# Kernel optimization log

Measured on AMD Instinct MI355X. Metric: run time of the kernel, lower is better.

Reference implementation:

```python
import jax, jax.numpy as jnp
import numpy as np

H = 2048

def _lstm_layer(x, W_ih, W_hh, b_ih, b_hh):
    # x: [B,T,I]; W_ih: [4H,I]; W_hh: [4H,H]; gate order i,f,g,o (PyTorch)
    B = x.shape[0]
    x_proj = jnp.einsum('bti,gi->btg', x, W_ih) + b_ih + b_hh  # [B,T,4H]
    def step(carry, xt):
        h, c = carry
        gates = xt + h @ W_hh.T                     # [B,4H]
        i, f, g, o = jnp.split(gates, 4, axis=-1)
        i = jax.nn.sigmoid(i); f = jax.nn.sigmoid(f)
        g = jnp.tanh(g);       o = jax.nn.sigmoid(o)
        c = f * c + i * g
        h = o * jnp.tanh(c)
        return (h, c), h
    h0 = jnp.zeros((B, H), x.dtype)
    c0 = jnp.zeros((B, H), x.dtype)
    _, ys = jax.lax.scan(step, (h0, c0), x_proj.transpose(1, 0, 2))
    return ys.transpose(1, 0, 2)  # [B,T,H]

def setup_inputs() -> dict:
    key = jax.random.key(0)
    ks = jax.random.split(key, 16)
    B, T, I, O = 16, 128, 128, 1
    s = 1.0 / np.sqrt(H)
    def u(k, shape):
        return jax.random.uniform(k, shape, jnp.float32, -s, s)
    inp = {"x": jax.random.normal(ks[0], (B, T, I), jnp.float32)}
    in_dims = [I, H, H]
    for l in range(3):
        inp[f"W_ih{l}"] = u(ks[1 + 4 * l], (4 * H, in_dims[l]))
        inp[f"W_hh{l}"] = u(ks[2 + 4 * l], (4 * H, H))
        inp[f"b_ih{l}"] = u(ks[3 + 4 * l], (4 * H,))
        inp[f"b_hh{l}"] = u(ks[4 + 4 * l], (4 * H,))
    inp["W_out"] = u(ks[13], (O, H))
    inp["b_out"] = u(ks[14], (O,))
    return inp

def reference(x, W_ih0, W_hh0, b_ih0, b_hh0,
              W_ih1, W_hh1, b_ih1, b_hh1,
              W_ih2, W_hh2, b_ih2, b_hh2,
              W_out, b_out):
    h = _lstm_layer(x, W_ih0, W_hh0, b_ih0, b_hh0)
    h = _lstm_layer(h, W_ih1, W_hh1, b_ih1, b_hh1)
    h = _lstm_layer(h, W_ih2, W_hh2, b_ih2, b_hh2)
    return h @ W_out.T + b_out  # [B,T,O]
```

## Files before the change

### kernel.cpp

```cpp
#include <hip/hip_runtime.h>
#include <hip/hip_fp16.h>
#include <cstdint>
#include <cstddef>


typedef __attribute__((ext_vector_type(8))) _Float16 fp16x8;
typedef __attribute__((ext_vector_type(4))) float    f32x4;

#define HDIM  2048
#define GATES 8192
#define BATCH 16
#define TSEQ  128
#define NTOK  2048
#define RED_ST 17
#define HSLOT 128
#define HSTEP_ELEMS 32768
#define FLAG_STRIDE 16
#define NFLAG_COPY 4
#define FB_OFF (NFLAG_COPY * 256 * FLAG_STRIDE)

union HU { _Float16 f; unsigned short u; };

__device__ __forceinline__ float sigmoidf_(float x) { return 1.f / (1.f + __expf(-x)); }
__device__ __forceinline__ float tanhf_(float x) {
    float e2 = __expf(2.f * x);
    return 1.f - 2.f / (e2 + 1.f);
}

__global__ __launch_bounds__(256) void cvt_f32_f16_kernel(const float* __restrict__ in,
                                                          _Float16* __restrict__ out, int n8) {
    int i = blockIdx.x * 256 + threadIdx.x;
    if (i >= n8) return;
    const float4* p = (const float4*)in + (size_t)i * 2;
    float4 a = p[0], b = p[1];
    fp16x8 v;
    v[0] = (_Float16)a.x; v[1] = (_Float16)a.y; v[2] = (_Float16)a.z; v[3] = (_Float16)a.w;
    v[4] = (_Float16)b.x; v[5] = (_Float16)b.y; v[6] = (_Float16)b.z; v[7] = (_Float16)b.w;
    ((fp16x8*)out)[i] = v;
}

__global__ __launch_bounds__(256) void xproj_gemm_kernel(
        const _Float16* __restrict__ A, const _Float16* __restrict__ Ah,
        const _Float16* __restrict__ W,
        const float* __restrict__ bih, const float* __restrict__ bhh,
        float* __restrict__ xp, int K) {
    __shared__ _Float16 As[128 * 64];
    __shared__ _Float16 Bs[128 * 64];
    const int tid  = threadIdx.x;
    const int lane = tid & 63;
    const int wave = tid >> 6;
    const int n0 = blockIdx.x * 128;
    const int m0 = blockIdx.y * 128;
    const int srow = tid >> 3;
    const int scol = (tid & 7) * 8;
    const int wr = (wave >> 1) * 64;
    const int wc = (wave & 1) * 64;
    const int lr = lane & 15;
    const int lk = (lane >> 4) * 8;

    f32x4 acc[4][4] = {};

    const int nk = K >> 6;
    for (int kt = 0; kt < nk; ++kt) {
        if (kt) __syncthreads();
        const int k0 = kt * 64;
#pragma unroll
        for (int cc = 0; cc < 4; ++cc) {
            const int row = cc * 32 + srow;
            const _Float16* ga;
            if (Ah) {
                const int m = m0 + row, b = m >> 7, tt = m & 127;
                ga = Ah + (size_t)(tt + 1) * HSTEP_ELEMS + (size_t)(k0 + scol) * 16 + b * 8;
            } else {
                ga = A + (size_t)(m0 + row) * K + k0 + scol;
            }
            const _Float16* gb = W + (size_t)(n0 + row) * K + k0 + scol;
            __builtin_amdgcn_global_load_lds(
                (const __attribute__((address_space(1))) void*)ga,
                (__attribute__((address_space(3))) void*)(As + cc * 2048 + wave * 512), 16, 0, 0);
            __builtin_amdgcn_global_load_lds(
                (const __attribute__((address_space(1))) void*)gb,
                (__attribute__((address_space(3))) void*)(Bs + cc * 2048 + wave * 512), 16, 0, 0);
        }
        __syncthreads();
#pragma unroll
        for (int s = 0; s < 2; ++s) {
            fp16x8 af[4], bf[4];
#pragma unroll
            for (int mi = 0; mi < 4; ++mi)
                af[mi] = *(const fp16x8*)(As + (wr + mi * 16 + lr) * 64 + s * 32 + lk);
#pragma unroll
            for (int ni = 0; ni < 4; ++ni)
                bf[ni] = *(const fp16x8*)(Bs + (wc + ni * 16 + lr) * 64 + s * 32 + lk);
#pragma unroll
            for (int mi = 0; mi < 4; ++mi)
#pragma unroll
                for (int ni = 0; ni < 4; ++ni)
                    acc[mi][ni] = __builtin_amdgcn_mfma_f32_16x16x32_f16(
                        af[mi], bf[ni], acc[mi][ni], 0, 0, 0);
        }
    }
    const int rb = (lane >> 4) * 4;
#pragma unroll
    for (int ni = 0; ni < 4; ++ni) {
        const int n = n0 + wc + ni * 16 + lr;
        const float bias = bih[n] + bhh[n];
#pragma unroll
        for (int mi = 0; mi < 4; ++mi) {
#pragma unroll
            for (int r = 0; r < 4; ++r) {
                const int m = m0 + wr + mi * 16 + rb + r;
                const int b = m >> 7, t = m & 127;
                xp[((size_t)t * BATCH + b) * GATES + n] = acc[mi][ni][r] + bias;
            }
        }
    }
}

__global__ __launch_bounds__(256, 1) void lstm_scan_kernel(
        const float* __restrict__ Whh,
        const float* __restrict__ xp,
        _Float16* __restrict__ hstep,
        int* __restrict__ flags,
        int flag_base) {
    __builtin_amdgcn_fence(__ATOMIC_ACQUIRE, "agent");

    __shared__ float red[2][8 * 16 * RED_ST];

    const int tid  = threadIdx.x;
    const int lane = tid & 63;
    const int wave = tid >> 6;
    const int blk  = blockIdx.x;
    const int h0   = blk * 8;
    const int ln15 = lane & 15;
    const int kl   = (lane >> 4) * 8;
    const int kbase = wave * 512;

    const int rq = ln15 >> 3, rj = ln15 & 7;
    const float* w0 = Whh + ((size_t)rq * HDIM + h0 + rj) * HDIM;
    const float* w1 = Whh + ((size_t)(rq + 2) * HDIM + h0 + rj) * HDIM;
    fp16x8 b0[16], b1[16];
#pragma unroll
    for (int s = 0; s < 16; ++s) {
        const int k = kbase + s * 32 + kl;
        float4 a0 = *(const float4*)(w0 + k), a1 = *(const float4*)(w0 + k + 4);
        float4 c0 = *(const float4*)(w1 + k), c1 = *(const float4*)(w1 + k + 4);
        fp16x8 v;
        v[0] = (_Float16)a0.x; v[1] = (_Float16)a0.y; v[2] = (_Float16)a0.z; v[3] = (_Float16)a0.w;
        v[4] = (_Float16)a1.x; v[5] = (_Float16)a1.y; v[6] = (_Float16)a1.z; v[7] = (_Float16)a1.w;
        b0[s] = v;
        v[0] = (_Float16)c0.x; v[1] = (_Float16)c0.y; v[2] = (_Float16)c0.z; v[3] = (_Float16)c0.w;
        v[4] = (_Float16)c1.x; v[5] = (_Float16)c1.y; v[6] = (_Float16)c1.z; v[7] = (_Float16)c1.w;
        b1[s] = v;
    }
    float c_state = 0.f;
    const int uh = tid & 7, ub = tid >> 3;

    const int pidx = ((blk & 3) << 8) | (wave << 6) | lane;
    const int* fa = flags + (size_t)pidx * FLAG_STRIDE;
    const int* fb = fa + FB_OFF;

    __syncthreads();

    for (int t = 0; t < TSEQ; ++t) {
        if (t) {
            while (__hip_atomic_load(fa, __ATOMIC_RELAXED, __HIP_MEMORY_SCOPE_AGENT) < flag_base + t ||
                   __hip_atomic_load(fb, __ATOMIC_RELAXED, __HIP_MEMORY_SCOPE_AGENT) < flag_base + t) {}
        }
        asm volatile("" ::: "memory");
        const _Float16* hsrc = hstep + (size_t)t * HSTEP_ELEMS;

        fp16x8 af[16];
#pragma unroll
        for (int s = 0; s < 16; ++s) {
            const int k = kbase + s * 32 + kl;
            af[s] = *(const fp16x8*)(hsrc + (size_t)k * 16 + ln15 * 8);
        }

        float xi = 0.f, xf = 0.f, xg = 0.f, xo = 0.f;
        if (tid < 128) {
            const float* xpt = xp + ((size_t)t * BATCH + ub) * GATES + h0 + uh;
            xi = xpt[0];
            xf = xpt[HDIM];
            xg = xpt[2 * HDIM];
            xo = xpt[3 * HDIM];
        }

        f32x4 a0e = {0.f,0.f,0.f,0.f}, a0o = {0.f,0.f,0.f,0.f};
        f32x4 a1e = {0.f,0.f,0.f,0.f}, a1o = {0.f,0.f,0.f,0.f};
#pragma unroll
        for (int s = 0; s < 16; s += 2) {
            a0e = __builtin_amdgcn_mfma_f32_16x16x32_f16(af[s],     b0[s],     a0e, 0, 0, 0);
            a1e = __builtin_amdgcn_mfma_f32_16x16x32_f16(af[s],     b1[s],     a1e, 0, 0, 0);
            a0o = __builtin_amdgcn_mfma_f32_16x16x32_f16(af[s + 1], b0[s + 1], a0o, 0, 0, 0);
            a1o = __builtin_amdgcn_mfma_f32_16x16x32_f16(af[s + 1], b1[s + 1], a1o, 0, 0, 0);
        }
        f32x4 acc0 = a0e + a0o;
        f32x4 acc1 = a1e + a1o;
        {
            float* r0 = red[t & 1] + ((wave * 2 + 0) * 16 + ln15) * RED_ST + (lane >> 4) * 4;
            float* r1 = red[t & 1] + ((wave * 2 + 1) * 16 + ln15) * RED_ST + (lane >> 4) * 4;
#pragma unroll
            for (int i = 0; i < 4; ++i) { r0[i] = acc0[i]; r1[i] = acc1[i]; }
        }
        __syncthreads();
        asm volatile("" ::: "memory");

        if (tid < 128) {
            const float* redp = red[t & 1];
            float ip = xi, fp_ = xf, gp = xg, op = xo;
#pragma unroll
            for (int w = 0; w < 4; ++w) {
                ip  += redp[((w * 2 + 0) * 16 + uh    ) * RED_ST + ub];
                fp_ += redp[((w * 2 + 0) * 16 + uh + 8) * RED_ST + ub];
                gp  += redp[((w * 2 + 1) * 16 + uh    ) * RED_ST + ub];
                op  += redp[((w * 2 + 1) * 16 + uh + 8) * RED_ST + ub];
            }
            float ig = sigmoidf_(ip), fg = sigmoidf_(fp_), og = sigmoidf_(op);
            float gg = tanhf_(gp);
            c_state = fg * c_state + ig * gg;
            float hv = og * tanhf_(c_state);
            HU cv; cv.f = (_Float16)hv;
            unsigned v  = cv.u;
            unsigned v1 = __shfl_down(v, 1, 64);
            unsigned v2 = __shfl_down(v, 2, 64);
            unsigned v3 = __shfl_down(v, 3, 64);
            if ((tid & 3) == 0) {
                unsigned long long pk = (unsigned long long)v
                                      | ((unsigned long long)v1 << 16)
                                      | ((unsigned long long)v2 << 32)
                                      | ((unsigned long long)v3 << 48);
                unsigned long long* dst = (unsigned long long*)
                    (hstep + (size_t)(t + 1) * HSTEP_ELEMS + blk * HSLOT + ub * 8 + uh);
                __hip_atomic_store(dst, pk, __ATOMIC_RELAXED, __HIP_MEMORY_SCOPE_AGENT);
            }
            if (t < TSEQ - 1) {
                asm volatile("s_waitcnt vmcnt(0)" ::: "memory");
                if (lane == 0) {
                    int* base = flags + (wave ? FB_OFF : 0);
#pragma unroll
                    for (int c = 0; c < NFLAG_COPY; ++c)
                        __hip_atomic_store(base + (size_t)((c << 8) | blk) * FLAG_STRIDE,
                                           flag_base + t + 1,
                                           __ATOMIC_RELAXED, __HIP_MEMORY_SCOPE_AGENT);
                }
            }
        }
    }
}

__global__ __launch_bounds__(256) void outproj_kernel(
        const _Float16* __restrict__ hstep, const float* __restrict__ Wout,
        const float* __restrict__ bout, float* __restrict__ out) {
    const int lane = threadIdx.x & 63;
    const int wave = threadIdx.x >> 6;
    const int tok = blockIdx.x * 4 + wave;
    const int b = tok >> 7, t = tok & 127;
    const _Float16* h = hstep + (size_t)(t + 1) * HSTEP_ELEMS + b * 8;
    float acc = 0.f;
#pragma unroll
    for (int c = 0; c < 4; ++c) {
        const int k = c * 512 + lane * 8;
        fp16x8 hv = *(const fp16x8*)(h + (size_t)k * 16);
        const float* w = Wout + k;
#pragma unroll
        for (int i = 0; i < 8; ++i) acc += (float)hv[i] * w[i];
    }
#pragma unroll
    for (int off = 32; off > 0; off >>= 1) acc += __shfl_down(acc, off, 64);
    if (lane == 0) out[tok] = acc + bout[0];
}

extern "C" void kernel_launch(void* const* d_in, const int* in_sizes, int n_in,
                              void* d_out, int out_size, void* d_ws, size_t ws_size,
                              hipStream_t stream) {
    (void)in_sizes; (void)n_in; (void)out_size; (void)ws_size;
    const float* x       = (const float*)d_in[0];
    const float* Wih[3]  = {(const float*)d_in[1], (const float*)d_in[5], (const float*)d_in[9]};
    const float* Whh[3]  = {(const float*)d_in[2], (const float*)d_in[6], (const float*)d_in[10]};
    const float* bih[3]  = {(const float*)d_in[3], (const float*)d_in[7], (const float*)d_in[11]};
    const float* bhh[3]  = {(const float*)d_in[4], (const float*)d_in[8], (const float*)d_in[12]};
    const float* Wout    = (const float*)d_in[13];
    const float* bout    = (const float*)d_in[14];
    float* out = (float*)d_out;

    char* ws = (char*)d_ws;
    size_t off = 0;
    auto carve = [&](size_t bytes) {
        char* p = ws + off;
        off += (bytes + 255) & ~(size_t)255;
        return p;
    };
    _Float16* wih16 = (_Float16*)carve((size_t)GATES * 2048 * 2);
    float*    xp    = (float*)   carve((size_t)TSEQ * GATES * BATCH * 4);
    _Float16* xh    = (_Float16*)carve((size_t)NTOK * 128 * 2);
    _Float16* hstep = (_Float16*)carve((size_t)(TSEQ + 1) * HSTEP_ELEMS * 2);
    int*      flags = (int*)     carve((size_t)2 * NFLAG_COPY * 256 * FLAG_STRIDE * 4);

    hipMemsetAsync(flags, 0, (size_t)2 * NFLAG_COPY * 256 * FLAG_STRIDE * 4, stream);
    hipMemsetAsync(hstep, 0, HSTEP_ELEMS * 2, stream);

    {
        int n8 = NTOK * 128 / 8;
        cvt_f32_f16_kernel<<<(n8 + 255) / 256, 256, 0, stream>>>(x, xh, n8);
    }

    const int Kl[3] = {128, 2048, 2048};
    for (int l = 0; l < 3; ++l) {
        int n8 = GATES * Kl[l] / 8;
        cvt_f32_f16_kernel<<<(n8 + 255) / 256, 256, 0, stream>>>(Wih[l], wih16, n8);
        dim3 ggrid(GATES / 128, NTOK / 128);
        xproj_gemm_kernel<<<ggrid, 256, 0, stream>>>(
            l == 0 ? xh : nullptr, l == 0 ? nullptr : hstep,
            wih16, bih[l], bhh[l], xp, Kl[l]);
        lstm_scan_kernel<<<256, 256, 0, stream>>>(Whh[l], xp, hstep, flags, l * TSEQ);
    }
    outproj_kernel<<<NTOK / 4, 256, 0, stream>>>(hstep, Wout, bout, out);
}
```

Measured before the change: 1.728 ms.

## Replace flag-based step barrier with sentinel-filled hidden-state ring polling

Drops the separate per-block flag counters and the vmcnt wait before the flag stores. Consumers now poll the hidden-state data directly: each 64-bit chunk is pre-filled with an fp16 infinity sentinel and reloaded until it is overwritten. This removes a store-to-flag round trip on every timestep of the serial recurrence. In exchange it adds a ring prefill kernel per layer, alternates two ring buffers between layers, and assumes a real h value never equals the sentinel.

Result: slower. 2.252 ms (+30.3%).

```diff
diff --git a/kernel.cpp b/kernel.cpp
--- a/kernel.cpp
+++ b/kernel.cpp
@@ -5,6 +5,7 @@
 
 
 typedef __attribute__((ext_vector_type(8))) _Float16 fp16x8;
+typedef __attribute__((ext_vector_type(4))) _Float16 fp16x4;
 typedef __attribute__((ext_vector_type(4))) float    f32x4;
 
 #define HDIM  2048
@@ -15,16 +16,26 @@
 #define RED_ST 17
 #define HSLOT 128
 #define HSTEP_ELEMS 32768
-#define FLAG_STRIDE 16
-#define NFLAG_COPY 4
-#define FB_OFF (NFLAG_COPY * 256 * FLAG_STRIDE)
-
+#define SLOT_ULL 8192
+#define RING_ULL ((size_t)(TSEQ + 1) * SLOT_ULL)
+#define SENT16 0x7C00u
+#define SENT64 0x7C007C007C007C00ULL
+
+union U8 { unsigned long long u; fp16x4 h4; };
 union HU { _Float16 f; unsigned short u; };
 
 __device__ __forceinline__ float sigmoidf_(float x) { return 1.f / (1.f + __expf(-x)); }
 __device__ __forceinline__ float tanhf_(float x) {
     float e2 = __expf(2.f * x);
     return 1.f - 2.f / (e2 + 1.f);
+}
+
+__global__ __launch_bounds__(256) void fill_rings_kernel(unsigned long long* __restrict__ p,
+                                                         int nring) {
+    size_t i = (size_t)blockIdx.x * 256 + threadIdx.x;
+    if (i >= (size_t)nring * RING_ULL) return;
+    size_t r = i % RING_ULL;
+    p[i] = (r < SLOT_ULL) ? 0ULL : SENT64;
 }
 
 __global__ __launch_bounds__(256) void cvt_f32_f16_kernel(const float* __restrict__ in,
@@ -120,9 +131,7 @@
 __global__ __launch_bounds__(256, 1) void lstm_scan_kernel(
         const float* __restrict__ Whh,
         const float* __restrict__ xp,
-        _Float16* __restrict__ hstep,
-        int* __restrict__ flags,
-        int flag_base) {
+        _Float16* __restrict__ ring) {
     __builtin_amdgcn_fence(__ATOMIC_ACQUIRE, "agent");
 
     __shared__ float red[2][8 * 16 * RED_ST];
@@ -153,30 +162,27 @@
         v[4] = (_Float16)c1.x; v[5] = (_Float16)c1.y; v[6] = (_Float16)c1.z; v[7] = (_Float16)c1.w;
         b1[s] = v;
     }
+#pragma unroll
+    for (int s = 0; s < 16; ++s) {
+        asm volatile("" : "+v"(b0[s]));
+        asm volatile("" : "+v"(b1[s]));
+    }
+
     float c_state = 0.f;
     const int uh = tid & 7, ub = tid >> 3;
-
-    const int pidx = ((blk & 3) << 8) | (wave << 6) | lane;
-    const int* fa = flags + (size_t)pidx * FLAG_STRIDE;
-    const int* fb = fa + FB_OFF;
-
+    unsigned long long* ringu = (unsigned long long*)ring;
+    const int kb0 = (kbase >> 3) + (kl >> 3);
     __syncthreads();
 
     for (int t = 0; t < TSEQ; ++t) {
-        if (t) {
-            while (__hip_atomic_load(fa, __ATOMIC_RELAXED, __HIP_MEMORY_SCOPE_AGENT) < flag_base + t ||
-                   __hip_atomic_load(fb, __ATOMIC_RELAXED, __HIP_MEMORY_SCOPE_AGENT) < flag_base + t) {}
-        }
-        asm volatile("" ::: "memory");
-        const _Float16* hsrc = hstep + (size_t)t * HSTEP_ELEMS;
-
-        fp16x8 af[16];
+        const unsigned long long* hp =
+            ringu + (size_t)t * SLOT_ULL + (size_t)kb0 * 32 + ln15 * 2;
+        unsigned long long lo[16], hi[16];
 #pragma unroll
         for (int s = 0; s < 16; ++s) {
-            const int k = kbase + s * 32 + kl;
-            af[s] = *(const fp16x8*)(hsrc + (size_t)k * 16 + ln15 * 8);
-        }
-
+            lo[s] = __hip_atomic_load(hp + s * 128,     __ATOMIC_RELAXED, __HIP_MEMORY_SCOPE_AGENT);
+            hi[s] = __hip_atomic_load(hp + s * 128 + 1, __ATOMIC_RELAXED, __HIP_MEMORY_SCOPE_AGENT);
+        }
         float xi = 0.f, xf = 0.f, xg = 0.f, xo = 0.f;
         if (tid < 128) {
             const float* xpt = xp + ((size_t)t * BATCH + ub) * GATES + h0 + uh;
@@ -185,15 +191,39 @@
             xg = xpt[2 * HDIM];
             xo = xpt[3 * HDIM];
         }
+        while (true) {
+            unsigned bad = 0;
+#pragma unroll
+            for (int s = 0; s < 16; ++s) {
+                if ((unsigned)(lo[s] & 0xFFFFu) == SENT16) bad |= 1u << (2 * s);
+                if ((unsigned)(hi[s] & 0xFFFFu) == SENT16) bad |= 1u << (2 * s + 1);
+            }
+            if (!bad) break;
+#pragma unroll
+            for (int s = 0; s < 16; ++s) {
+                if (bad & (1u << (2 * s)))
+                    lo[s] = __hip_atomic_load(hp + s * 128,     __ATOMIC_RELAXED, __HIP_MEMORY_SCOPE_AGENT);
+                if (bad & (1u << (2 * s + 1)))
+                    hi[s] = __hip_atomic_load(hp + s * 128 + 1, __ATOMIC_RELAXED, __HIP_MEMORY_SCOPE_AGENT);
+            }
+        }
 
         f32x4 a0e = {0.f,0.f,0.f,0.f}, a0o = {0.f,0.f,0.f,0.f};
         f32x4 a1e = {0.f,0.f,0.f,0.f}, a1o = {0.f,0.f,0.f,0.f};
 #pragma unroll
         for (int s = 0; s < 16; s += 2) {
-            a0e = __builtin_amdgcn_mfma_f32_16x16x32_f16(af[s],     b0[s],     a0e, 0, 0, 0);
-            a1e = __builtin_amdgcn_mfma_f32_16x16x32_f16(af[s],     b1[s],     a1e, 0, 0, 0);
-            a0o = __builtin_amdgcn_mfma_f32_16x16x32_f16(af[s + 1], b0[s + 1], a0o, 0, 0, 0);
-            a1o = __builtin_amdgcn_mfma_f32_16x16x32_f16(af[s + 1], b1[s + 1], a1o, 0, 0, 0);
+            U8 L0, H0, L1, H1;
+            L0.u = lo[s];     H0.u = hi[s];
+            L1.u = lo[s + 1]; H1.u = hi[s + 1];
+            fp16x8 ae, ao;
+            ae[0]=L0.h4[0]; ae[1]=L0.h4[1]; ae[2]=L0.h4[2]; ae[3]=L0.h4[3];
+            ae[4]=H0.h4[0]; ae[5]=H0.h4[1]; ae[6]=H0.h4[2]; ae[7]=H0.h4[3];
+            ao[0]=L1.h4[0]; ao[1]=L1.h4[1]; ao[2]=L1.h4[2]; ao[3]=L1.h4[3];
+            ao[4]=H1.h4[0]; ao[5]=H1.h4[1]; ao[6]=H1.h4[2]; ao[7]=H1.h4[3];
+            a0e = __builtin_amdgcn_mfma_f32_16x16x32_f16(ae, b0[s],     a0e, 0, 0, 0);
+            a1e = __builtin_amdgcn_mfma_f32_16x16x32_f16(ae, b1[s],     a1e, 0, 0, 0);
+            a0o = __builtin_amdgcn_mfma_f32_16x16x32_f16(ao, b0[s + 1], a0o, 0, 0, 0);
+            a1o = __builtin_amdgcn_mfma_f32_16x16x32_f16(ao, b1[s + 1], a1o, 0, 0, 0);
         }
         f32x4 acc0 = a0e + a0o;
         f32x4 acc1 = a1e + a1o;
@@ -230,33 +260,22 @@
                                       | ((unsigned long long)v1 << 16)
                                       | ((unsigned long long)v2 << 32)
                                       | ((unsigned long long)v3 << 48);
-                unsigned long long* dst = (unsigned long long*)
-                    (hstep + (size_t)(t + 1) * HSTEP_ELEMS + blk * HSLOT + ub * 8 + uh);
+                unsigned long long* dst =
+                    ringu + (size_t)(t + 1) * SLOT_ULL + blk * 32 + ub * 2 + (uh >> 2);
                 __hip_atomic_store(dst, pk, __ATOMIC_RELAXED, __HIP_MEMORY_SCOPE_AGENT);
             }
-            if (t < TSEQ - 1) {
-                asm volatile("s_waitcnt vmcnt(0)" ::: "memory");
-                if (lane == 0) {
-                    int* base = flags + (wave ? FB_OFF : 0);
-#pragma unroll
-                    for (int c = 0; c < NFLAG_COPY; ++c)
-                        __hip_atomic_store(base + (size_t)((c << 8) | blk) * FLAG_STRIDE,
-                                           flag_base + t + 1,
-                                           __ATOMIC_RELAXED, __HIP_MEMORY_SCOPE_AGENT);
-                }
-            }
         }
     }
 }
 
 __global__ __launch_bounds__(256) void outproj_kernel(
-        const _Float16* __restrict__ hstep, const float* __restrict__ Wout,
+        const _Float16* __restrict__ ring, const float* __restrict__ Wout,
         const float* __restrict__ bout, float* __restrict__ out) {
     const int lane = threadIdx.x & 63;
     const int wave = threadIdx.x >> 6;
     const int tok = blockIdx.x * 4 + wave;
     const int b = tok >> 7, t = tok & 127;
-    const _Float16* h = hstep + (size_t)(t + 1) * HSTEP_ELEMS + b * 8;
+    const _Float16* h = ring + (size_t)(t + 1) * HSTEP_ELEMS + b * 8;
     float acc = 0.f;
 #pragma unroll
     for (int c = 0; c < 4; ++c) {
@@ -294,26 +313,35 @@
     _Float16* wih16 = (_Float16*)carve((size_t)GATES * 2048 * 2);
     float*    xp    = (float*)   carve((size_t)TSEQ * GATES * BATCH * 4);
     _Float16* xh    = (_Float16*)carve((size_t)NTOK * 128 * 2);
-    _Float16* hstep = (_Float16*)carve((size_t)(TSEQ + 1) * HSTEP_ELEMS * 2);
-    int*      flags = (int*)     carve((size_t)2 * NFLAG_COPY * 256 * FLAG_STRIDE * 4);
-
-    hipMemsetAsync(flags, 0, (size_t)2 * NFLAG_COPY * 256 * FLAG_STRIDE * 4, stream);
-    hipMemsetAsync(hstep, 0, HSTEP_ELEMS * 2, stream);
-
+    _Float16* rings = (_Float16*)carve(2 * RING_ULL * 8);
+    _Float16* ring0 = rings;
+    _Float16* ring1 = rings + RING_ULL * 4;
+
+    {
+        size_t nw = 2 * RING_ULL;
+        fill_rings_kernel<<<(unsigned)((nw + 255) / 256), 256, 0, stream>>>(
+            (unsigned long long*)rings, 2);
+    }
     {
         int n8 = NTOK * 128 / 8;
         cvt_f32_f16_kernel<<<(n8 + 255) / 256, 256, 0, stream>>>(x, xh, n8);
     }
 
+    _Float16* ringL[3]  = {ring0, ring1, ring0};
     const int Kl[3] = {128, 2048, 2048};
     for (int l = 0; l < 3; ++l) {
         int n8 = GATES * Kl[l] / 8;
         cvt_f32_f16_kernel<<<(n8 + 255) / 256, 256, 0, stream>>>(Wih[l], wih16, n8);
         dim3 ggrid(GATES / 128, NTOK / 128);
         xproj_gemm_kernel<<<ggrid, 256, 0, stream>>>(
-            l == 0 ? xh : nullptr, l == 0 ? nullptr : hstep,
+            l == 0 ? xh : nullptr, l == 0 ? nullptr : ringL[l - 1],
             wih16, bih[l], bhh[l], xp, Kl[l]);
-        lstm_scan_kernel<<<256, 256, 0, stream>>>(Whh[l], xp, hstep, flags, l * TSEQ);
-    }
-    outproj_kernel<<<NTOK / 4, 256, 0, stream>>>(hstep, Wout, bout, out);
-}
+        if (l == 2) {
+            size_t nw = RING_ULL;
+            fill_rings_kernel<<<(unsigned)((nw + 255) / 256), 256, 0, stream>>>(
+                (unsigned long long*)ring0, 1);
+        }
+        lstm_scan_kernel<<<256, 256, 0, stream>>>(Whh[l], xp, ringL[l]);
+    }
+    outproj_kernel<<<NTOK / 4, 256, 0, stream>>>(ringL[2], Wout, bout, out);
+}
```
